# Kernel tuning notes

Measured on AMD Instinct MI355X. Metric: run time of the kernel, lower is better.

Reference implementation:

```python
import jax, jax.numpy as jnp
import numpy as np

B, N, M, D, HEADS, L, DFF, TSTEPS = 8, 1024, 512, 128, 8, 6, 512, 100
S = N + M
HD = D // HEADS


def _layer_norm(x, g, b):
    mu = jnp.mean(x, axis=-1, keepdims=True)
    var = jnp.var(x, axis=-1, keepdims=True)
    return (x - mu) * jax.lax.rsqrt(var + 1e-5) * g + b


def setup_inputs() -> dict:
    rng = np.random.default_rng(0)
    # sparse parity-check matrix, ~6 ones per check row
    H = (rng.random((M, N)) < 6.0 / N).astype(np.float32)
    # create_mask with n_rings=1: eye(S) plus variable<->check Tanner edges
    conn = np.eye(S, dtype=np.float32)
    conn[N:, :N] = np.maximum(conn[N:, :N], H)
    conn[:N, N:] = np.maximum(conn[:N, N:], H.T)
    mask = ~(conn > 0)  # True = attention blocked (src_mask semantics)

    key = jax.random.key(0)
    ks = jax.random.split(key, 16)
    s = 0.05  # weight init scale ~ 1/sqrt(d_model)
    return {
        "r_t": jax.random.normal(ks[0], (B, N), jnp.float32),
        "t": jax.random.randint(ks[1], (B,), 0, TSTEPS),
        "pcm": jnp.asarray(H.astype(np.int32)),
        "mask": jnp.asarray(mask),
        "src_embed": jax.random.uniform(ks[2], (S, D), jnp.float32),
        "time_table": jax.random.normal(ks[3], (TSTEPS, D), jnp.float32),
        "Wq": jax.random.normal(ks[4], (L, D, D), jnp.float32) * s,
        "Wk": jax.random.normal(ks[5], (L, D, D), jnp.float32) * s,
        "Wv": jax.random.normal(ks[6], (L, D, D), jnp.float32) * s,
        "Wo": jax.random.normal(ks[7], (L, D, D), jnp.float32) * s,
        "W1": jax.random.normal(ks[8], (L, D, DFF), jnp.float32) * s,
        "W2": jax.random.normal(ks[9], (L, DFF, D), jnp.float32) * s,
        "g1": jnp.ones((L, D), jnp.float32),
        "b1": jnp.zeros((L, D), jnp.float32),
        "g2": jnp.ones((L, D), jnp.float32),
        "b2": jnp.zeros((L, D), jnp.float32),
        "fc_w": jax.random.normal(ks[10], (D, 1), jnp.float32) * s,
        "fc_b": jnp.zeros((1,), jnp.float32),
    }


def reference(r_t, t, pcm, mask, src_embed, time_table, Wq, Wk, Wv, Wo,
              W1, W2, g1, b1, g2, b2, fc_w, fc_b):
    # to_bin: BPSK sign -> bit {0,1}
    bits = 0.5 * (1.0 - jnp.sign(r_t))                       # [B, N]
    syn = (bits @ pcm.T.astype(jnp.float32)) % 2.0           # mod-2 syndrome [B, M]
    nodes = jnp.concatenate([jnp.abs(r_t), syn], axis=-1)    # [B, S]
    x = src_embed[None, :, :] * nodes[:, :, None]            # [B, S, D]
    te = time_table[t]                                       # [B, D] time embedding
    x = te[:, None, :] * x                                   # time-modulated input
    bias = jnp.where(mask, -1e9, 0.0)[None, None]            # [1, 1, S, S]
    inv_sqrt_hd = 1.0 / jnp.sqrt(jnp.float32(HD))
    for l in range(L):
        h = _layer_norm(x, g1[l], b1[l])
        q = (h @ Wq[l]).reshape(B, S, HEADS, HD)
        k = (h @ Wk[l]).reshape(B, S, HEADS, HD)
        v = (h @ Wv[l]).reshape(B, S, HEADS, HD)
        scores = jnp.einsum('bqhd,bkhd->bhqk', q, k) * inv_sqrt_hd + bias
        p = jax.nn.softmax(scores, axis=-1)
        o = jnp.einsum('bhqk,bkhd->bqhd', p, v).reshape(B, S, D)
        x = x + o @ Wo[l]
        # FiLM-style time conditioning on the FFN branch
        h2 = _layer_norm(x, g2[l], b2[l]) * te[:, None, :]
        x = x + jax.nn.relu(h2 @ W1[l]) @ W2[l]
    return x @ fc_w + fc_b                                   # z_hat [B, S, 1]
```

## Files before the change

kernel.cpp:

```cpp
#include <hip/hip_runtime.h>
#include <cmath>
#include <cstdint>

constexpr int B_ = 8, N_ = 1024, M_ = 512, D_ = 128, S_ = 1536, L_ = 6, DFF_ = 512;
constexpr int ROWS = B_ * S_;
constexpr int MAXDEG = 64;
constexpr int LKEY = 32;
constexpr int RPB  = 48;
constexpr int NBLK = ROWS / RPB;
constexpr int BPB  = S_ / RPB;
constexpr int NTILE = 12;
constexpr int TILE  = 128 * 128;

typedef __bf16 bf16x8 __attribute__((ext_vector_type(8)));
typedef float  f32x4  __attribute__((ext_vector_type(4)));
typedef unsigned short u16x8 __attribute__((ext_vector_type(8)));

__device__ inline unsigned short f2bf(float f) {
  unsigned u = __float_as_uint(f);
  u += 0x7fffu + ((u >> 16) & 1u);
  return (unsigned short)(u >> 16);
}
__device__ inline float bf2f(unsigned short u) {
  return __uint_as_float(((unsigned)u) << 16);
}
__device__ inline void ull2f4(unsigned long long u, float* f) {
  f[0] = bf2f((unsigned short)(u));
  f[1] = bf2f((unsigned short)(u >> 16));
  f[2] = bf2f((unsigned short)(u >> 32));
  f[3] = bf2f((unsigned short)(u >> 48));
}

__device__ __forceinline__ void async_ld16(const unsigned short* g, unsigned short* l) {
  __builtin_amdgcn_global_load_lds(
      (const __attribute__((address_space(1))) unsigned int*)(uintptr_t)g,
      (__attribute__((address_space(3))) unsigned int*)(unsigned)(uintptr_t)l,
      16, 0, 0);
}
__device__ __forceinline__ void issue_tile(const unsigned short* tp, unsigned short* bs,
                                           int w, int lane) {
  for (int c = w; c < 32; c += 6)
    async_ld16(tp + c * 512 + lane * 8, bs + c * 512);
}

__global__ void adj_init(int* __restrict__ adj, int* __restrict__ adjcnt) {
  int s = blockIdx.x * blockDim.x + threadIdx.x;
  if (s < S_) { adj[s * MAXDEG] = s; adjcnt[s] = 1; }
}
__global__ void adj_build(const int* __restrict__ pcm, int* __restrict__ adj,
                          int* __restrict__ adjcnt) {
  int c = blockIdx.x;
  int lane = threadIdx.x;
  const int* row = pcm + c * N_;
  for (int base = 0; base < N_; base += 64) {
    int k = base + lane;
    if (row[k] != 0) {
      int s1 = atomicAdd(&adjcnt[N_ + c], 1);
      if (s1 < MAXDEG) adj[(N_ + c) * MAXDEG + s1] = k;
      int s2 = atomicAdd(&adjcnt[k], 1);
      if (s2 < MAXDEG) adj[k * MAXDEG + s2] = N_ + c;
    }
  }
}

__global__ void xinit_kernel(const float* __restrict__ r_t, const int* __restrict__ adj,
                             const int* __restrict__ adjcnt, const float* __restrict__ se,
                             const int* __restrict__ tt, const float* __restrict__ table,
                             float* __restrict__ x, unsigned* __restrict__ barrier_cnt) {
  int bs = blockIdx.x;
  int b = bs / S_, s = bs % S_;
  int d = threadIdx.x;
  if (bs < 8 && d == 0)
    __hip_atomic_store(barrier_cnt + bs * 32, 0u, __ATOMIC_RELAXED, __HIP_MEMORY_SCOPE_AGENT);
  float node;
  if (s < N_) {
    node = fabsf(r_t[b * N_ + s]);
  } else {
    int cnt = adjcnt[s]; cnt = cnt < MAXDEG ? cnt : MAXDEG;
    float sum = 0.f;
    for (int j = 0; j < cnt; ++j) {
      int k = adj[s * MAXDEG + j];
      if (k < N_) {
        float r = r_t[b * N_ + k];
        sum += (r < 0.f) ? 1.f : (r > 0.f ? 0.f : 0.5f);
      }
    }
    node = fmodf(sum, 2.0f);
  }
  x[(size_t)bs * D_ + d] = table[tt[b] * D_ + d] * se[s * D_ + d] * node;
}

constexpr int WLAYER = NTILE * TILE;

__global__ void wconv_kernel(const float* __restrict__ Wq, const float* __restrict__ Wk,
                             const float* __restrict__ Wv, const float* __restrict__ Wo,
                             const float* __restrict__ W1, const float* __restrict__ W2,
                             unsigned short* __restrict__ out) {
  __shared__ unsigned short tl[128 * 130];
  int bid = blockIdx.x;
  int l = bid / NTILE, tile = bid % NTILE;
  const float* src;
  int rstride, coff = 0;
  if (tile == 0)      { src = Wk + (size_t)l * D_ * D_;  rstride = D_; }
  else if (tile == 1) { src = Wv + (size_t)l * D_ * D_;  rstride = D_; }
  else if (tile == 2) { src = Wq + (size_t)l * D_ * D_;  rstride = D_; }
  else if (tile == 3) { src = Wo + (size_t)l * D_ * D_;  rstride = D_; }
  else {
    int c = (tile - 4) >> 1;
    if (((tile - 4) & 1) == 0) { src = W1 + (size_t)l * D_ * DFF_; rstride = DFF_; coff = c * 128; }
    else                       { src = W2 + (size_t)l * DFF_ * D_ + (size_t)c * 128 * D_; rstride = D_; }
  }
  for (int i = threadIdx.x; i < 16384; i += 256) {
    int kd = i >> 7, rr = i & 127;
    tl[kd * 130 + rr] = f2bf(src[(size_t)kd * rstride + coff + rr]);
  }
  __syncthreads();
  unsigned short* o = out + (size_t)bid * TILE;
  for (int i = threadIdx.x; i < 16384; i += 256) {
    int rr = i >> 7;
    int sw = (i >> 3) & 15, e = i & 7;
    int kd = (sw ^ (rr & 15)) * 8 + e;
    o[i] = tl[kd * 130 + rr];
  }
}

__device__ __forceinline__ void mfma4(const unsigned short* As, const unsigned short* Bs,
                                      int rowbase, int colbase, int quad, int l16,
                                      f32x4 (&acc)[4]) {
#pragma unroll
  for (int kk = 0; kk < 4; ++kk) {
    int cb = kk * 4 + quad;
    int row = rowbase + l16;
    bf16x8 a = __builtin_bit_cast(bf16x8, *(const uint4*)&As[row * 128 + ((cb ^ (row & 15)) << 3)]);
    bf16x8 bb[4];
#pragma unroll
    for (int ct = 0; ct < 4; ++ct) {
      int n = colbase + ct * 16 + l16;
      bb[ct] = __builtin_bit_cast(bf16x8, *(const uint4*)&Bs[n * 128 + ((cb ^ (n & 15)) << 3)]);
    }
#pragma unroll
    for (int ct = 0; ct < 4; ++ct)
      acc[ct] = __builtin_amdgcn_mfma_f32_16x16x32_bf16(a, bb[ct], acc[ct], 0, 0, 0);
  }
}

__device__ __forceinline__ void grid_barrier(unsigned* cnt, unsigned target) {
  __syncthreads();
  if (threadIdx.x == 0) {
    __hip_atomic_fetch_add(cnt, 1u, __ATOMIC_RELAXED, __HIP_MEMORY_SCOPE_AGENT);
    while (__hip_atomic_load(cnt, __ATOMIC_RELAXED, __HIP_MEMORY_SCOPE_AGENT) < target)
      __builtin_amdgcn_s_sleep(4);
  }
  __syncthreads();
}

__global__ void __launch_bounds__(384) mega_kernel(
    const float* __restrict__ x0, unsigned short* __restrict__ kv0,
    unsigned short* __restrict__ kv1, const unsigned short* __restrict__ wbf,
    const float* __restrict__ g1, const float* __restrict__ b1,
    const float* __restrict__ g2, const float* __restrict__ b2,
    const int* __restrict__ tt, const float* __restrict__ table,
    const int* __restrict__ adj, const int* __restrict__ adjc,
    const float* __restrict__ fcw, const float* __restrict__ fcb,
    float* __restrict__ out, unsigned* barrier_cnt) {
  __shared__ unsigned short As[RPB * 128];
  __shared__ unsigned short Bs[3][TILE];
  __shared__ unsigned short Cs[RPB * 128];
  __shared__ unsigned short KVs[RPB * 256];
  __shared__ float red1[2][RPB], red2[2][RPB];
  __shared__ int sKeys[RPB * LKEY];
  __shared__ int sCnt[RPB];
  const int row0 = blockIdx.x * RPB;
  const int b = row0 / S_;
  const int bS = b * S_;
  const int t = threadIdx.x, w = t >> 6, lane = t & 63, quad = lane >> 4, l16 = lane & 15;
  const int wr = w >> 1, wc = w & 1;
  const int rowbase = wr * 16, colbase = wc * 64;
  const int tbase = tt[b] * D_;
  unsigned* bcnt = barrier_cnt + b * 32;

  issue_tile(wbf + 0 * TILE, Bs[0], w, lane);
  issue_tile(wbf + 1 * TILE, Bs[1], w, lane);
  issue_tile(wbf + 2 * TILE, Bs[2], w, lane);

  f32x4 xreg[4];
#pragma unroll
  for (int ct = 0; ct < 4; ++ct)
#pragma unroll
    for (int i = 0; i < 4; ++i) {
      int row = row0 + rowbase + quad * 4 + i;
      int col = colbase + ct * 16 + l16;
      xreg[ct][i] = x0[(size_t)row * D_ + col];
    }
  if (t < RPB) {
    int c = adjc[row0 + t - bS];
    sCnt[t] = c < MAXDEG ? c : MAXDEG;
  }
  for (int i = t; i < RPB * LKEY; i += 384) {
    int r = i / LKEY, j = i % LKEY;
    sKeys[i] = adj[(row0 + r - bS) * MAXDEG + j];
  }

  for (int l = 0; l < L_; ++l) {
    const unsigned short* wt = wbf + (size_t)l * WLAYER;
    const float* g1l = g1 + l * D_;
    const float* b1l = b1 + l * D_;
    const float* g2l = g2 + l * D_;
    const float* b2l = b2 + l * D_;
    unsigned short* kv = (l & 1) ? kv1 : kv0;

    float mu1[4], rs1[4];
#pragma unroll
    for (int i = 0; i < 4; ++i) {
      float s = 0.f, sq = 0.f;
#pragma unroll
      for (int ct = 0; ct < 4; ++ct) { s += xreg[ct][i]; sq += xreg[ct][i] * xreg[ct][i]; }
      for (int off = 1; off < 16; off <<= 1) { s += __shfl_xor(s, off); sq += __shfl_xor(sq, off); }
      if (l16 == 0) { red1[wc][rowbase + quad * 4 + i] = s; red2[wc][rowbase + quad * 4 + i] = sq; }
    }
    __syncthreads();
#pragma unroll
    for (int i = 0; i < 4; ++i) {
      int r = rowbase + quad * 4 + i;
      float mu = (red1[0][r] + red1[1][r]) * (1.f / 128.f);
      float var = (red2[0][r] + red2[1][r]) * (1.f / 128.f) - mu * mu;
      mu1[i] = mu;
      rs1[i] = rsqrtf(var + 1e-5f);
    }
#pragma unroll
    for (int ct = 0; ct < 4; ++ct)
#pragma unroll
      for (int i = 0; i < 4; ++i) {
        int rowL = rowbase + quad * 4 + i;
        int col = colbase + ct * 16 + l16;
        float h = (xreg[ct][i] - mu1[i]) * rs1[i] * g1l[col] + b1l[col];
        As[rowL * 128 + (((col >> 3) ^ (rowL & 15)) << 3) + (col & 7)] = f2bf(h);
      }
    __syncthreads();

    {
      f32x4 acc[4];
#pragma unroll
      for (int j = 0; j < 4; ++j) acc[j] = f32x4{0.f, 0.f, 0.f, 0.f};
      mfma4(As, Bs[0], rowbase, colbase, quad, l16, acc);
#pragma unroll
      for (int ct = 0; ct < 4; ++ct)
#pragma unroll
        for (int i = 0; i < 4; ++i) {
          int rowL = rowbase + quad * 4 + i;
          KVs[rowL * 256 + colbase + ct * 16 + l16] = f2bf(acc[ct][i]);
        }
    }
    {
      f32x4 acc[4];
#pragma unroll
      for (int j = 0; j < 4; ++j) acc[j] = f32x4{0.f, 0.f, 0.f, 0.f};
      mfma4(As, Bs[1], rowbase, colbase, quad, l16, acc);
#pragma unroll
      for (int ct = 0; ct < 4; ++ct)
#pragma unroll
        for (int i = 0; i < 4; ++i) {
          int rowL = rowbase + quad * 4 + i;
          KVs[rowL * 256 + 128 + colbase + ct * 16 + l16] = f2bf(acc[ct][i]);
        }
    }
    {
      f32x4 acc[4];
#pragma unroll
      for (int j = 0; j < 4; ++j) acc[j] = f32x4{0.f, 0.f, 0.f, 0.f};
      mfma4(As, Bs[2], rowbase, colbase, quad, l16, acc);
#pragma unroll
      for (int ct = 0; ct < 4; ++ct)
#pragma unroll
        for (int i = 0; i < 4; ++i) {
          int rowL = rowbase + quad * 4 + i;
          int col = colbase + ct * 16 + l16;
          Cs[rowL * 128 + (((col >> 3) ^ (rowL & 15)) << 3) + (col & 7)] = f2bf(acc[ct][i]);
        }
    }
    __syncthreads();
    for (int i = t; i < RPB * 128; i += 384) {
      int rL = i >> 7, cw = i & 127;
      unsigned u = *(const unsigned*)&KVs[rL * 256 + cw * 2];
      __hip_atomic_store((unsigned*)&kv[(size_t)(row0 + rL) * 256 + cw * 2],
                         u, __ATOMIC_RELAXED, __HIP_MEMORY_SCOPE_AGENT);
    }

    grid_barrier(bcnt, (unsigned)(BPB * (l + 1)));

    issue_tile(wt + 3 * TILE, Bs[0], w, lane);
    issue_tile(wt + 4 * TILE, Bs[1], w, lane);
    issue_tile(wt + 5 * TILE, Bs[2], w, lane);

    {
      const int rL = t >> 3, h = t & 7;
      const int s = row0 + rL - bS;
      const int cnt = sCnt[rL];
      float q[16];
      {
        u16x8 qa = *(const u16x8*)&Cs[rL * 128 + (((2 * h) ^ (rL & 15)) << 3)];
        u16x8 qb = *(const u16x8*)&Cs[rL * 128 + (((2 * h + 1) ^ (rL & 15)) << 3)];
#pragma unroll
        for (int j = 0; j < 8; ++j) { q[j] = bf2f(qa[j]); q[8 + j] = bf2f(qb[j]); }
      }
      float m = -1e30f, lsum = 0.f;
      float o16[16];
#pragma unroll
      for (int j = 0; j < 16; ++j) o16[j] = 0.f;
      for (int jb = 0; jb < cnt; jb += 4) {
        unsigned long long K[4][4], V[4][4];
#pragma unroll
        for (int u = 0; u < 4; ++u) {
          int j = jb + u;
          int key = 0;
          if (j < cnt) key = (j < LKEY) ? sKeys[rL * LKEY + j] : adj[s * MAXDEG + j];
          const unsigned long long* kp =
              (const unsigned long long*)(kv + (size_t)(bS + key) * 256 + h * 16);
#pragma unroll
          for (int c = 0; c < 4; ++c) {
            K[u][c] = __hip_atomic_load(kp + c, __ATOMIC_RELAXED, __HIP_MEMORY_SCOPE_AGENT);
            V[u][c] = __hip_atomic_load(kp + 32 + c, __ATOMIC_RELAXED, __HIP_MEMORY_SCOPE_AGENT);
          }
        }
#pragma unroll
        for (int u = 0; u < 4; ++u) {
          float kf[16], vf[16];
#pragma unroll
          for (int c = 0; c < 4; ++c) { ull2f4(K[u][c], kf + 4 * c); ull2f4(V[u][c], vf + 4 * c); }
          float dot = 0.f;
#pragma unroll
          for (int j = 0; j < 16; ++j) dot = fmaf(q[j], kf[j], dot);
          dot *= 0.25f;
          if (jb + u >= cnt) dot = -1e30f;
          const float mn = fmaxf(m, dot);
          const float rescale = __expf(m - mn);
          const float e = __expf(dot - mn);
          lsum = lsum * rescale + e;
#pragma unroll
          for (int j = 0; j < 16; ++j) o16[j] = o16[j] * rescale + e * vf[j];
          m = mn;
        }
      }
      const float inv = 1.f / lsum;
      u16x8 pk0, pk1;
#pragma unroll
      for (int j = 0; j < 8; ++j) {
        pk0[j] = f2bf(o16[j] * inv);
        pk1[j] = f2bf(o16[8 + j] * inv);
      }
      *(u16x8*)&As[rL * 128 + (((2 * h) ^ (rL & 15)) << 3)] = pk0;
      *(u16x8*)&As[rL * 128 + (((2 * h + 1) ^ (rL & 15)) << 3)] = pk1;
    }
    __syncthreads();

    f32x4 acc1[4];
#pragma unroll
    for (int j = 0; j < 4; ++j) acc1[j] = f32x4{0.f, 0.f, 0.f, 0.f};
    mfma4(As, Bs[0], rowbase, colbase, quad, l16, acc1);
    f32x4 xp[4];
#pragma unroll
    for (int ct = 0; ct < 4; ++ct)
#pragma unroll
      for (int i = 0; i < 4; ++i) xp[ct][i] = xreg[ct][i] + acc1[ct][i];
    float mu_[4], rs_[4];
#pragma unroll
    for (int i = 0; i < 4; ++i) {
      float s = 0.f, sq = 0.f;
#pragma unroll
      for (int ct = 0; ct < 4; ++ct) { s += xp[ct][i]; sq += xp[ct][i] * xp[ct][i]; }
      for (int off = 1; off < 16; off <<= 1) { s += __shfl_xor(s, off); sq += __shfl_xor(sq, off); }
      if (l16 == 0) { red1[wc][rowbase + quad * 4 + i] = s; red2[wc][rowbase + quad * 4 + i] = sq; }
    }
    __syncthreads();
#pragma unroll
    for (int i = 0; i < 4; ++i) {
      int r = rowbase + quad * 4 + i;
      float mu = (red1[0][r] + red1[1][r]) * (1.f / 128.f);
      float var = (red2[0][r] + red2[1][r]) * (1.f / 128.f) - mu * mu;
      mu_[i] = mu;
      rs_[i] = rsqrtf(var + 1e-5f);
    }
#pragma unroll
    for (int ct = 0; ct < 4; ++ct)
#pragma unroll
      for (int i = 0; i < 4; ++i) {
        int rowL = rowbase + quad * 4 + i;
        int col = colbase + ct * 16 + l16;
        float h2 = (xp[ct][i] - mu_[i]) * rs_[i] * g2l[col] + b2l[col];
        h2 *= table[tbase + col];
        As[rowL * 128 + (((col >> 3) ^ (rowL & 15)) << 3) + (col & 7)] = f2bf(h2);
      }
    __syncthreads();

    f32x4 acc2[4];
#pragma unroll
    for (int j = 0; j < 4; ++j) acc2[j] = f32x4{0.f, 0.f, 0.f, 0.f};
    const int bufW1[4] = {1, 0, 2, 1};
    const int bufW2[4] = {2, 1, 0, 2};
#pragma unroll
    for (int c = 0; c < 4; ++c) {
      f32x4 accF[4];
#pragma unroll
      for (int j = 0; j < 4; ++j) accF[j] = f32x4{0.f, 0.f, 0.f, 0.f};
      mfma4(As, Bs[bufW1[c]], rowbase, colbase, quad, l16, accF);
#pragma unroll
      for (int ct = 0; ct < 4; ++ct)
#pragma unroll
        for (int i = 0; i < 4; ++i) {
          int rowL = rowbase + quad * 4 + i;
          int col = colbase + ct * 16 + l16;
          Cs[rowL * 128 + (((col >> 3) ^ (rowL & 15)) << 3) + (col & 7)] =
              f2bf(fmaxf(accF[ct][i], 0.f));
        }
      __syncthreads();
      if (c < 3) issue_tile(wt + (4 + 2 * (c + 1)) * TILE, Bs[bufW1[c + 1]], w, lane);
      else if (l < L_ - 1) issue_tile(wt + WLAYER + 0 * TILE, Bs[0], w, lane);
      mfma4(Cs, Bs[bufW2[c]], rowbase, colbase, quad, l16, acc2);
      __syncthreads();
      if (c < 3) issue_tile(wt + (5 + 2 * (c + 1)) * TILE, Bs[bufW2[c + 1]], w, lane);
      else if (l < L_ - 1) {
        issue_tile(wt + WLAYER + 1 * TILE, Bs[1], w, lane);
        issue_tile(wt + WLAYER + 2 * TILE, Bs[2], w, lane);
      }
    }
    if (l < L_ - 1) {
#pragma unroll
      for (int ct = 0; ct < 4; ++ct)
#pragma unroll
        for (int i = 0; i < 4; ++i) xreg[ct][i] = xp[ct][i] + acc2[ct][i];
    } else {
      float pr[4] = {0.f, 0.f, 0.f, 0.f};
#pragma unroll
      for (int ct = 0; ct < 4; ++ct)
#pragma unroll
        for (int i = 0; i < 4; ++i)
          pr[i] += (xp[ct][i] + acc2[ct][i]) * fcw[colbase + ct * 16 + l16];
#pragma unroll
      for (int i = 0; i < 4; ++i) {
        float s = pr[i];
        for (int off = 1; off < 16; off <<= 1) s += __shfl_xor(s, off);
        if (l16 == 0) red1[wc][rowbase + quad * 4 + i] = s;
      }
      __syncthreads();
      if (wc == 0 && l16 == 0)
#pragma unroll
        for (int i = 0; i < 4; ++i) {
          int r = rowbase + quad * 4 + i;
          out[row0 + r] = red1[0][r] + red1[1][r] + fcb[0];
        }
    }
  }
}

extern "C" void kernel_launch(void* const* d_in, const int* in_sizes, int n_in,
                              void* d_out, int out_size, void* d_ws, size_t ws_size,
                              hipStream_t stream) {
  const float* r_t       = (const float*)d_in[0];
  const int*   t         = (const int*)d_in[1];
  const int*   pcm       = (const int*)d_in[2];
  const float* src_embed = (const float*)d_in[4];
  const float* time_tab  = (const float*)d_in[5];
  const float* Wq = (const float*)d_in[6];
  const float* Wk = (const float*)d_in[7];
  const float* Wv = (const float*)d_in[8];
  const float* Wo = (const float*)d_in[9];
  const float* W1 = (const float*)d_in[10];
  const float* W2 = (const float*)d_in[11];
  const float* g1 = (const float*)d_in[12];
  const float* b1 = (const float*)d_in[13];
  const float* g2 = (const float*)d_in[14];
  const float* b2 = (const float*)d_in[15];
  const float* fc_w = (const float*)d_in[16];
  const float* fc_b = (const float*)d_in[17];
  float* out = (float*)d_out;

  char* ws = (char*)d_ws;
  size_t off = 0;
  auto alloc = [&](size_t bytes) -> void* {
    void* p = ws + off;
    off = (off + bytes + 255) & ~(size_t)255;
    return p;
  };
  float*          x    = (float*)alloc((size_t)ROWS * D_ * 4);
  unsigned short* kv0  = (unsigned short*)alloc((size_t)ROWS * 256 * 2);
  unsigned short* kv1  = (unsigned short*)alloc((size_t)ROWS * 256 * 2);
  int*            adj  = (int*)alloc((size_t)S_ * MAXDEG * 4);
  int*            adjc = (int*)alloc((size_t)S_ * 4);
  unsigned short* wbf  = (unsigned short*)alloc((size_t)L_ * WLAYER * 2);
  unsigned*       bcnt = (unsigned*)alloc(8 * 32 * 4);

  adj_init<<<(S_ + 255) / 256, 256, 0, stream>>>(adj, adjc);
  adj_build<<<M_, 64, 0, stream>>>(pcm, adj, adjc);
  wconv_kernel<<<L_ * NTILE, 256, 0, stream>>>(Wq, Wk, Wv, Wo, W1, W2, wbf);
  xinit_kernel<<<ROWS, 128, 0, stream>>>(r_t, adj, adjc, src_embed, t, time_tab, x, bcnt);

  mega_kernel<<<NBLK, 384, 0, stream>>>(x, kv0, kv1, wbf, g1, b1, g2, b2,
                                        t, time_tab, adj, adjc, fc_w, fc_b, out, bcnt);
}
```

Baseline: 286.6 us.

## Use per-layer KV buffers and plain 16-byte vector loads in sparse attention

Gives each layer its own K/V buffer instead of ping-ponging two buffers. Because no buffer is rewritten while another block may still be reading it, the gather can drop the relaxed atomic 8-byte loads and use ordinary 16-byte vector loads that the compiler can cache and combine. The cost is six times the KV workspace. Once the loads are non-atomic, correctness depends on the grid barrier plus cache visibility at agent scope; stale L1/L2 data across CUs is a possible risk.

```diff
diff --git a/kernel.cpp b/kernel.cpp
--- a/kernel.cpp
+++ b/kernel.cpp
@@ -11,6 +11,7 @@
 constexpr int BPB  = S_ / RPB;
 constexpr int NTILE = 12;
 constexpr int TILE  = 128 * 128;
+constexpr int KVSZ  = ROWS * 256;
 
 typedef __bf16 bf16x8 __attribute__((ext_vector_type(8)));
 typedef float  f32x4  __attribute__((ext_vector_type(4)));
@@ -23,12 +24,6 @@
 }
 __device__ inline float bf2f(unsigned short u) {
   return __uint_as_float(((unsigned)u) << 16);
-}
-__device__ inline void ull2f4(unsigned long long u, float* f) {
-  f[0] = bf2f((unsigned short)(u));
-  f[1] = bf2f((unsigned short)(u >> 16));
-  f[2] = bf2f((unsigned short)(u >> 32));
-  f[3] = bf2f((unsigned short)(u >> 48));
 }
 
 __device__ __forceinline__ void async_ld16(const unsigned short* g, unsigned short* l) {
@@ -155,8 +150,8 @@
 }
 
 __global__ void __launch_bounds__(384) mega_kernel(
-    const float* __restrict__ x0, unsigned short* __restrict__ kv0,
-    unsigned short* __restrict__ kv1, const unsigned short* __restrict__ wbf,
+    const float* __restrict__ x0, unsigned short* __restrict__ kvbase,
+    const unsigned short* __restrict__ wbf,
     const float* __restrict__ g1, const float* __restrict__ b1,
     const float* __restrict__ g2, const float* __restrict__ b2,
     const int* __restrict__ tt, const float* __restrict__ table,
@@ -207,7 +202,7 @@
     const float* b1l = b1 + l * D_;
     const float* g2l = g2 + l * D_;
     const float* b2l = b2 + l * D_;
-    unsigned short* kv = (l & 1) ? kv1 : kv0;
+    unsigned short* kv = kvbase + (size_t)l * KVSZ;
 
     float mu1[4], rs1[4];
 #pragma unroll
@@ -308,28 +303,24 @@
 #pragma unroll
       for (int j = 0; j < 16; ++j) o16[j] = 0.f;
       for (int jb = 0; jb < cnt; jb += 4) {
-        unsigned long long K[4][4], V[4][4];
+        u16x8 K[4][2], V[4][2];
 #pragma unroll
         for (int u = 0; u < 4; ++u) {
           int j = jb + u;
           int key = 0;
           if (j < cnt) key = (j < LKEY) ? sKeys[rL * LKEY + j] : adj[s * MAXDEG + j];
-          const unsigned long long* kp =
-              (const unsigned long long*)(kv + (size_t)(bS + key) * 256 + h * 16);
-#pragma unroll
-          for (int c = 0; c < 4; ++c) {
-            K[u][c] = __hip_atomic_load(kp + c, __ATOMIC_RELAXED, __HIP_MEMORY_SCOPE_AGENT);
-            V[u][c] = __hip_atomic_load(kp + 32 + c, __ATOMIC_RELAXED, __HIP_MEMORY_SCOPE_AGENT);
+          const u16x8* kp = (const u16x8*)(kv + (size_t)(bS + key) * 256 + h * 16);
+          K[u][0] = kp[0];  K[u][1] = kp[1];
+          V[u][0] = kp[16]; V[u][1] = kp[17];
+        }
+#pragma unroll
+        for (int u = 0; u < 4; ++u) {
+          float dot = 0.f;
+#pragma unroll
+          for (int j = 0; j < 8; ++j) {
+            dot = fmaf(q[j], bf2f(K[u][0][j]), dot);
+            dot = fmaf(q[8 + j], bf2f(K[u][1][j]), dot);
           }
-        }
-#pragma unroll
-        for (int u = 0; u < 4; ++u) {
-          float kf[16], vf[16];
-#pragma unroll
-          for (int c = 0; c < 4; ++c) { ull2f4(K[u][c], kf + 4 * c); ull2f4(V[u][c], vf + 4 * c); }
-          float dot = 0.f;
-#pragma unroll
-          for (int j = 0; j < 16; ++j) dot = fmaf(q[j], kf[j], dot);
           dot *= 0.25f;
           if (jb + u >= cnt) dot = -1e30f;
           const float mn = fmaxf(m, dot);
@@ -337,7 +328,10 @@
           const float e = __expf(dot - mn);
           lsum = lsum * rescale + e;
 #pragma unroll
-          for (int j = 0; j < 16; ++j) o16[j] = o16[j] * rescale + e * vf[j];
+          for (int j = 0; j < 8; ++j) {
+            o16[j]     = o16[j]     * rescale + e * bf2f(V[u][0][j]);
+            o16[8 + j] = o16[8 + j] * rescale + e * bf2f(V[u][1][j]);
+          }
           m = mn;
         }
       }
@@ -482,8 +476,7 @@
     return p;
   };
   float*          x    = (float*)alloc((size_t)ROWS * D_ * 4);
-  unsigned short* kv0  = (unsigned short*)alloc((size_t)ROWS * 256 * 2);
-  unsigned short* kv1  = (unsigned short*)alloc((size_t)ROWS * 256 * 2);
+  unsigned short* kv   = (unsigned short*)alloc((size_t)L_ * KVSZ * 2);
   int*            adj  = (int*)alloc((size_t)S_ * MAXDEG * 4);
   int*            adjc = (int*)alloc((size_t)S_ * 4);
   unsigned short* wbf  = (unsigned short*)alloc((size_t)L_ * WLAYER * 2);
@@ -494,6 +487,6 @@
   wconv_kernel<<<L_ * NTILE, 256, 0, stream>>>(Wq, Wk, Wv, Wo, W1, W2, wbf);
   xinit_kernel<<<ROWS, 128, 0, stream>>>(r_t, adj, adjc, src_embed, t, time_tab, x, bcnt);
 
-  mega_kernel<<<NBLK, 384, 0, stream>>>(x, kv0, kv1, wbf, g1, b1, g2, b2,
+  mega_kernel<<<NBLK, 384, 0, stream>>>(x, kv, wbf, g1, b1, g2, b2,
                                         t, time_tab, adj, adjc, fc_w, fc_b, out, bcnt);
 }
```

New measurement: 260.0 us. 1.1x faster.
